# Optimization experiments

Measured on AMD Instinct MI355X. Metric: run time of the kernel, lower is better.

Reference implementation:

```python
import jax, jax.numpy as jnp
import numpy as np

# Dims
B, S, D, N, K, NOPS = 4, 2048, 512, 16, 4, 4
NUM_LAYERS = 1
SCALE = 1.0 / float(np.sqrt(NUM_LAYERS))   # base_layer.residual_scale
GAMMA = 0.01                                # lindblad_gamma
COND_THRESH = 100.0                         # condition_threshold
MHC_ITERS, MHC_TAU = 10, 0.05


def setup_inputs() -> dict:
    key = jax.random.key(0)
    ks = jax.random.split(key, 16)
    def rn(k, shape, s=0.02):
        return jax.random.normal(k, shape, dtype=jnp.float32) * s
    return {
        "x_real": jax.random.normal(ks[0], (B, S, D), dtype=jnp.float32),
        "x_imag": jax.random.normal(ks[1], (B, S, D), dtype=jnp.float32),
        "Win_r": rn(ks[2], (D, D)), "Win_i": rn(ks[3], (D, D)),
        "conv_w": rn(ks[4], (K, D), 0.5),
        "W_dt": rn(ks[5], (D, D)), "b_dt": jnp.full((D,), -4.0, jnp.float32),
        "A_log": jnp.tile(jnp.log(jnp.arange(1, N + 1, dtype=jnp.float32)), (D, 1)),
        "W_B": rn(ks[6], (D, N)), "W_C": rn(ks[7], (D, N)),
        "D_skip": jnp.ones((D,), jnp.float32),
        "Wout_r": rn(ks[8], (D, D)), "Wout_i": rn(ks[9], (D, D)),
        "L_r": rn(ks[10], (NOPS, D), 0.1), "L_i": rn(ks[11], (NOPS, D), 0.1),
        "phi": rn(ks[12], (D,), 0.1),
        "H_res_logits": jnp.zeros((1, 1), jnp.float32),
        "H_res_logits_imag": jnp.zeros((1, 1), jnp.float32),
    }


def _causal_dwconv(u, w):
    # u: [B,S,D] complex, w: [K,D] real depthwise causal kernel
    Kk, Ss = w.shape[0], u.shape[1]
    up = jnp.pad(u, ((0, 0), (Kk - 1, 0), (0, 0)))
    return sum(w[k][None, None, :] * up[:, k:k + Ss, :] for k in range(Kk))


def _forward(x_real, x_imag, Win_r, Win_i, conv_w, W_dt, b_dt, A_log, W_B, W_C,
             D_skip, Wout_r, Wout_i, L_r, L_i, phi, H_res_logits, H_res_logits_imag):
    x = jax.lax.complex(x_real, x_imag)                       # [B,S,D] complex64
    # ---- base ComplexMamba3Layer: complex in-proj -> causal dwconv -> mod-gate -> selective scan -> out-proj ----
    u = x @ jax.lax.complex(Win_r, Win_i)
    u = _causal_dwconv(u, conv_w)
    u = u * jax.nn.sigmoid(jnp.abs(u)).astype(u.dtype)        # magnitude gate (modSiLU)
    xr = u.real
    dt = jax.nn.softplus(xr @ W_dt + b_dt)                    # [B,S,D]
    Bm = xr @ W_B                                             # [B,S,N]
    Cm = xr @ W_C                                             # [B,S,N]
    A = -jnp.exp(A_log)                                       # [D,N]
    def step(h, inp):
        dt_t, Bm_t, Cm_t, u_t = inp                            # [B,D],[B,N],[B,N],[B,D]c
        decay = jnp.exp(dt_t[..., None] * A).astype(h.dtype)  # [B,D,N]
        h = decay * h + (dt_t.astype(u_t.dtype) * u_t)[..., None] * Bm_t[:, None, :].astype(u_t.dtype)
        y_t = jnp.einsum('bdn,bn->bd', h, Cm_t.astype(h.dtype))
        return h, y_t
    h0 = jnp.zeros((x.shape[0], D, N), dtype=u.dtype)
    xs = (jnp.swapaxes(dt, 0, 1), jnp.swapaxes(Bm, 0, 1), jnp.swapaxes(Cm, 0, 1), jnp.swapaxes(u, 0, 1))
    _, ys = jax.lax.scan(step, h0, xs)
    y = jnp.swapaxes(ys, 0, 1) + D_skip.astype(u.dtype) * u
    y = y @ jax.lax.complex(Wout_r, Wout_i)
    out = x + SCALE * y
    # ---- V8 wrapper ----
    branch = (out - x) / max(SCALE, 1e-8)
    # Lindblad dissipation: psi * (1 - gamma * sum_k |L_k|^2), diagonal jump operators
    coeff = jnp.sum(L_r ** 2 + L_i ** 2, axis=0)              # [D]
    branch = branch * (1.0 - GAMMA * coeff).astype(branch.dtype)
    # approximate Hamiltonian (no-grad): H = (1/S) sum_s |psi_s><psi_s|
    mag = jnp.abs(branch)
    H = jax.lax.stop_gradient(jnp.einsum('bsd,bse->bde', mag, mag) / mag.shape[1])
    # hybrid automata: _H_prev is None on the first forward -> no jump applied (faithful to source)
    # quaternionic escape: condition proxy from H diagonal, phase rotation if singular
    diag = jnp.diagonal(H, axis1=1, axis2=2)                  # [B,D]
    cond = jnp.max(diag, axis=-1) / (jnp.min(diag, axis=-1) + 1e-8)
    escaped = cond > COND_THRESH                              # [B]
    rot = jnp.exp(jax.lax.complex(jnp.zeros_like(phi), phi))  # unit phase per dim
    branch = jnp.where(escaped[:, None, None], branch * rot, branch)
    branch = branch * SCALE
    # mHC residual: Sinkhorn on 1x1 logits (streams=1) with complex phase
    M = jnp.exp(H_res_logits / MHC_TAU)
    for _ in range(MHC_ITERS):
        M = M / jnp.sum(M, axis=1, keepdims=True)
        M = M / jnp.sum(M, axis=0, keepdims=True)
    coef = M[0, 0] * jnp.exp(jax.lax.complex(jnp.zeros(()), H_res_logits_imag[0, 0]))
    out = x + coef.astype(branch.dtype) * branch
    return jnp.stack([out.real, out.imag])                    # [2,B,S,D] real view


def reference(x_real, x_imag, Win_r, Win_i, conv_w, W_dt, b_dt, A_log, W_B, W_C,
              D_skip, Wout_r, Wout_i, L_r, L_i, phi, H_res_logits, H_res_logits_imag):
    return _forward(x_real, x_imag, Win_r, Win_i, conv_w, W_dt, b_dt, A_log, W_B, W_C,
                    D_skip, Wout_r, Wout_i, L_r, L_i, phi, H_res_logits, H_res_logits_imag)
```

## Files before the change

kernel.cpp:

```cpp
#include <hip/hip_runtime.h>
#include <math.h>

#define BB 4
#define SSEQ 2048
#define DDIM 512
#define NSTATE 16
#define KCONV 4
#define NOPS_ 4
#define GAMMA_ 0.01f
#define CONDT_ 100.0f
#define SCALE_ 1.0f
#define NC 128
#define LC 16

static const size_t BSD = (size_t)BB * SSEQ * DDIM;
static const size_t BSN = (size_t)BB * SSEQ * NSTATE;
static const size_t MIDSZ = (size_t)BB * NC * DDIM * NSTATE;

typedef short short8v __attribute__((ext_vector_type(8)));
typedef float f32x4 __attribute__((ext_vector_type(4)));

__device__ __forceinline__ short f2bf(float x) {
    union { float f; unsigned int u; } v; v.f = x;
    unsigned int u = v.u + 0x7FFFu + ((v.u >> 16) & 1u);
    return (short)(u >> 16);
}
__device__ __forceinline__ short8v cvt8(const float4 a, const float4 b) {
    short8v r;
    r[0] = f2bf(a.x); r[1] = f2bf(a.y); r[2] = f2bf(a.z); r[3] = f2bf(a.w);
    r[4] = f2bf(b.x); r[5] = f2bf(b.y); r[6] = f2bf(b.z); r[7] = f2bf(b.w);
    return r;
}

__global__ __launch_bounds__(256) void convert_weights(
    const float* __restrict__ W0, const float* __restrict__ W1,
    const float* __restrict__ W2, const float* __restrict__ W3,
    const float* __restrict__ W4,
    unsigned short* __restrict__ T0, unsigned short* __restrict__ T1,
    unsigned short* __restrict__ T2, unsigned short* __restrict__ T3,
    unsigned short* __restrict__ T4)
{
    __shared__ float tile[64][65];
    const int n0 = (blockIdx.x & 7) * 64, k0 = (blockIdx.x >> 3) * 64;
    const float* srcs[5] = {W0, W1, W2, W3, W4};
    unsigned short* dsts[5] = {T0, T1, T2, T3, T4};
    #pragma unroll
    for (int m = 0; m < 5; ++m) {
        const float* W = srcs[m];
        unsigned short* T = dsts[m];
        for (int it = 0; it < 16; ++it) {
            const int idx = it * 256 + threadIdx.x;
            const int r = idx >> 6, c = idx & 63;
            tile[r][c] = W[(size_t)(k0 + r) * DDIM + n0 + c];
        }
        __syncthreads();
        for (int it = 0; it < 16; ++it) {
            const int idx = it * 256 + threadIdx.x;
            const int r = idx >> 6, c = idx & 63;
            T[(size_t)(n0 + r) * DDIM + k0 + c] = (unsigned short)f2bf(tile[c][r]);
        }
        __syncthreads();
    }
}

__global__ __launch_bounds__(256) void convert_bc(
    const float* __restrict__ WB, const float* __restrict__ WC,
    unsigned short* __restrict__ WdtT)
{
    const int idx = blockIdx.x * 256 + threadIdx.x;
    const int r = idx >> 9;
    const int k = idx & 511;
    float v = 0.f;
    if (r < 16) v = WB[(size_t)k * NSTATE + r];
    else if (r < 32) v = WC[(size_t)k * NSTATE + (r - 16)];
    WdtT[(size_t)(512 + r) * DDIM + k] = (unsigned short)f2bf(v);
}

template <bool LIND>
__global__ __launch_bounds__(256, 4) void cgemm_mfma(
    const float* __restrict__ Ar, const float* __restrict__ Ai,
    const unsigned short* __restrict__ WTr, const unsigned short* __restrict__ WTi,
    const float* __restrict__ Lr, const float* __restrict__ Li,
    float* __restrict__ Cr, float* __restrict__ Ci)
{
    __shared__ unsigned short Ar_s[64 * 32], Ai_s[64 * 32];
    __shared__ unsigned short Br_s[64 * 32], Bi_s[64 * 32];
    const int q8 = (int)(gridDim.x >> 3);
    const int lg = (blockIdx.x & 7) * q8 + (blockIdx.x >> 3);
    const int col0 = (lg & 7) * 64;
    const int row0 = (lg >> 3) * 64;
    const int tid = threadIdx.x;
    const int lane = tid & 63, wave = tid >> 6;
    const int wm = wave >> 1, wn = wave & 1;
    const int srow = tid >> 2;
    const int q = tid & 3;

    f32x4 accr[2][2], acci[2][2];
    #pragma unroll
    for (int a = 0; a < 2; ++a)
        #pragma unroll
        for (int b = 0; b < 2; ++b) { accr[a][b] = (f32x4)0.f; acci[a][b] = (f32x4)0.f; }

    for (int k0 = 0; k0 < DDIM; k0 += 32) {
        {
            const size_t ab = (size_t)(row0 + srow) * DDIM + k0 + q * 8;
            const float4 r0 = *reinterpret_cast<const float4*>(Ar + ab);
            const float4 r1 = *reinterpret_cast<const float4*>(Ar + ab + 4);
            const float4 i0 = *reinterpret_cast<const float4*>(Ai + ab);
            const float4 i1 = *reinterpret_cast<const float4*>(Ai + ab + 4);
            const int ix = srow * 32 + ((q ^ ((srow >> 1) & 3)) << 3);
            *reinterpret_cast<short8v*>(&Ar_s[ix]) = cvt8(r0, r1);
            *reinterpret_cast<short8v*>(&Ai_s[ix]) = cvt8(i0, i1);
            const size_t wb = (size_t)(col0 + srow) * DDIM + k0 + q * 8;
            *reinterpret_cast<short8v*>(&Br_s[ix]) = *reinterpret_cast<const short8v*>(WTr + wb);
            *reinterpret_cast<short8v*>(&Bi_s[ix]) = *reinterpret_cast<const short8v*>(WTi + wb);
        }
        __syncthreads();
        short8v ar[2], ai[2], ain[2], wr[2], wi[2];
        const int ks = lane >> 4;
        #pragma unroll
        for (int mi = 0; mi < 2; ++mi) {
            const int r = wm * 32 + mi * 16 + (lane & 15);
            const int idx = r * 32 + ((ks ^ ((r >> 1) & 3)) << 3);
            ar[mi] = *reinterpret_cast<const short8v*>(&Ar_s[idx]);
            ai[mi] = *reinterpret_cast<const short8v*>(&Ai_s[idx]);
            #pragma unroll
            for (int j = 0; j < 8; ++j) ain[mi][j] = ai[mi][j] ^ (short)0x8000;
        }
        #pragma unroll
        for (int nj = 0; nj < 2; ++nj) {
            const int n = wn * 32 + nj * 16 + (lane & 15);
            const int idx = n * 32 + ((ks ^ ((n >> 1) & 3)) << 3);
            wr[nj] = *reinterpret_cast<const short8v*>(&Br_s[idx]);
            wi[nj] = *reinterpret_cast<const short8v*>(&Bi_s[idx]);
        }
        #pragma unroll
        for (int mi = 0; mi < 2; ++mi)
            #pragma unroll
            for (int nj = 0; nj < 2; ++nj) {
                accr[mi][nj] = __builtin_amdgcn_mfma_f32_16x16x32_bf16(ar[mi], wr[nj], accr[mi][nj], 0, 0, 0);
                accr[mi][nj] = __builtin_amdgcn_mfma_f32_16x16x32_bf16(ain[mi], wi[nj], accr[mi][nj], 0, 0, 0);
                acci[mi][nj] = __builtin_amdgcn_mfma_f32_16x16x32_bf16(ar[mi], wi[nj], acci[mi][nj], 0, 0, 0);
                acci[mi][nj] = __builtin_amdgcn_mfma_f32_16x16x32_bf16(ai[mi], wr[nj], acci[mi][nj], 0, 0, 0);
            }
        __syncthreads();
    }
    float lindv[2] = {1.f, 1.f};
    if (LIND) {
        #pragma unroll
        for (int nj = 0; nj < 2; ++nj) {
            const int col = col0 + wn * 32 + nj * 16 + (lane & 15);
            float s = 0.f;
            #pragma unroll
            for (int k = 0; k < NOPS_; ++k) {
                const float lr = Lr[k * DDIM + col], li = Li[k * DDIM + col];
                s += lr * lr + li * li;
            }
            lindv[nj] = 1.0f - GAMMA_ * s;
        }
    }
    #pragma unroll
    for (int mi = 0; mi < 2; ++mi)
        #pragma unroll
        for (int nj = 0; nj < 2; ++nj) {
            const int col = col0 + wn * 32 + nj * 16 + (lane & 15);
            #pragma unroll
            for (int rr = 0; rr < 4; ++rr) {
                const int row = row0 + wm * 32 + mi * 16 + (lane >> 4) * 4 + rr;
                Cr[(size_t)row * DDIM + col] = accr[mi][nj][rr] * lindv[nj];
                Ci[(size_t)row * DDIM + col] = acci[mi][nj][rr] * lindv[nj];
            }
        }
}

__global__ __launch_bounds__(256, 4) void rgemm_fused(
    const float* __restrict__ A, const unsigned short* __restrict__ WT,
    const float* __restrict__ bias, float* __restrict__ Out,
    float* __restrict__ Bm, float* __restrict__ Cm)
{
    __shared__ unsigned short A_s[64 * 32], B_s[64 * 32];
    const int q8 = (int)(gridDim.x >> 3);
    const int lg = (blockIdx.x & 7) * q8 + (blockIdx.x >> 3);
    const int col0 = (lg % 9) * 64;
    const int row0 = (lg / 9) * 64;
    const int tid = threadIdx.x;
    const int lane = tid & 63, wave = tid >> 6;
    const int wm = wave >> 1, wn = wave & 1;
    const int srow = tid >> 2, q = tid & 3;

    f32x4 acc[2][2];
    #pragma unroll
    for (int a = 0; a < 2; ++a)
        #pragma unroll
        for (int b = 0; b < 2; ++b) acc[a][b] = (f32x4)0.f;

    for (int k0 = 0; k0 < DDIM; k0 += 32) {
        {
            const size_t ab = (size_t)(row0 + srow) * DDIM + k0 + q * 8;
            const float4 r0 = *reinterpret_cast<const float4*>(A + ab);
            const float4 r1 = *reinterpret_cast<const float4*>(A + ab + 4);
            const int ix = srow * 32 + ((q ^ ((srow >> 1) & 3)) << 3);
            *reinterpret_cast<short8v*>(&A_s[ix]) = cvt8(r0, r1);
            const size_t wb = (size_t)(col0 + srow) * DDIM + k0 + q * 8;
            *reinterpret_cast<short8v*>(&B_s[ix]) = *reinterpret_cast<const short8v*>(WT + wb);
        }
        __syncthreads();
        short8v av[2], bv[2];
        const int ks = lane >> 4;
        #pragma unroll
        for (int mi = 0; mi < 2; ++mi) {
            const int r = wm * 32 + mi * 16 + (lane & 15);
            av[mi] = *reinterpret_cast<const short8v*>(&A_s[r * 32 + ((ks ^ ((r >> 1) & 3)) << 3)]);
        }
        #pragma unroll
        for (int nj = 0; nj < 2; ++nj) {
            const int n = wn * 32 + nj * 16 + (lane & 15);
            bv[nj] = *reinterpret_cast<const short8v*>(&B_s[n * 32 + ((ks ^ ((n >> 1) & 3)) << 3)]);
        }
        #pragma unroll
        for (int mi = 0; mi < 2; ++mi)
            #pragma unroll
            for (int nj = 0; nj < 2; ++nj)
                acc[mi][nj] = __builtin_amdgcn_mfma_f32_16x16x32_bf16(av[mi], bv[nj], acc[mi][nj], 0, 0, 0);
        __syncthreads();
    }
    #pragma unroll
    for (int mi = 0; mi < 2; ++mi)
        #pragma unroll
        for (int nj = 0; nj < 2; ++nj) {
            const int col = col0 + wn * 32 + nj * 16 + (lane & 15);
            if (col < 512) {
                const float bz = bias[col];
                #pragma unroll
                for (int rr = 0; rr < 4; ++rr) {
                    const int row = row0 + wm * 32 + mi * 16 + (lane >> 4) * 4 + rr;
                    const float z = acc[mi][nj][rr] + bz;
                    Out[(size_t)row * DDIM + col] =
                        (z > 0.f) ? (z + __logf(1.f + __expf(-z))) : __logf(1.f + __expf(z));
                }
            } else if (col < 528) {
                #pragma unroll
                for (int rr = 0; rr < 4; ++rr) {
                    const int row = row0 + wm * 32 + mi * 16 + (lane >> 4) * 4 + rr;
                    Bm[(size_t)row * NSTATE + (col - 512)] = acc[mi][nj][rr];
                }
            } else if (col < 544) {
                #pragma unroll
                for (int rr = 0; rr < 4; ++rr) {
                    const int row = row0 + wm * 32 + mi * 16 + (lane >> 4) * 4 + rr;
                    Cm[(size_t)row * NSTATE + (col - 528)] = acc[mi][nj][rr];
                }
            }
        }
}

__global__ __launch_bounds__(256) void conv_gate_kernel(
    const float* __restrict__ ur, const float* __restrict__ ui,
    const float* __restrict__ w, float* __restrict__ gr, float* __restrict__ gi)
{
    const size_t idx = ((size_t)blockIdx.x * 256 + threadIdx.x) * 4;
    const int d = (int)(idx % DDIM);
    const int s = (int)((idx / DDIM) % SSEQ);
    float4 ar = {0.f, 0.f, 0.f, 0.f}, ai = {0.f, 0.f, 0.f, 0.f};
    #pragma unroll
    for (int k = 0; k < KCONV; ++k) {
        const int soff = s + k - (KCONV - 1);
        if (soff >= 0) {
            const size_t j = idx + (size_t)((long)(k - (KCONV - 1)) * DDIM);
            const float4 wk = *reinterpret_cast<const float4*>(w + k * DDIM + d);
            const float4 u4 = *reinterpret_cast<const float4*>(ur + j);
            const float4 v4 = *reinterpret_cast<const float4*>(ui + j);
            ar.x += wk.x * u4.x; ar.y += wk.y * u4.y; ar.z += wk.z * u4.z; ar.w += wk.w * u4.w;
            ai.x += wk.x * v4.x; ai.y += wk.y * v4.y; ai.z += wk.z * v4.z; ai.w += wk.w * v4.w;
        }
    }
    float4 go_r, go_i;
    {
        const float m0 = sqrtf(ar.x * ar.x + ai.x * ai.x);
        const float m1 = sqrtf(ar.y * ar.y + ai.y * ai.y);
        const float m2 = sqrtf(ar.z * ar.z + ai.z * ai.z);
        const float m3 = sqrtf(ar.w * ar.w + ai.w * ai.w);
        const float s0 = 1.f / (1.f + __expf(-m0));
        const float s1 = 1.f / (1.f + __expf(-m1));
        const float s2 = 1.f / (1.f + __expf(-m2));
        const float s3 = 1.f / (1.f + __expf(-m3));
        go_r.x = ar.x * s0; go_r.y = ar.y * s1; go_r.z = ar.z * s2; go_r.w = ar.w * s3;
        go_i.x = ai.x * s0; go_i.y = ai.y * s1; go_i.z = ai.z * s2; go_i.w = ai.w * s3;
    }
    *reinterpret_cast<float4*>(gr + idx) = go_r;
    *reinterpret_cast<float4*>(gi + idx) = go_i;
}

__global__ __launch_bounds__(256) void scan_phase1(
    const float* __restrict__ dt, const float* __restrict__ gr, const float* __restrict__ gi,
    const float* __restrict__ Bm, const float* __restrict__ A_log,
    float* __restrict__ mid_hr, float* __restrict__ mid_hi, float* __restrict__ dtsum)
{
    __shared__ float bm_s[LC * NSTATE];
    const int blk = blockIdx.x;
    const int dblk = blk & 1;
    const int c = (blk >> 1) & (NC - 1);
    const int b = blk >> 8;
    const int tid = threadIdx.x;
    const int d = dblk * 256 + tid;
    const int s0 = c * LC;
    bm_s[tid] = Bm[((size_t)b * SSEQ + s0) * NSTATE + tid];
    float A_dn[16], hr[16], hi[16];
    #pragma unroll
    for (int n = 0; n < 16; ++n) {
        A_dn[n] = -__expf(A_log[d * NSTATE + n]);
        hr[n] = 0.f; hi[n] = 0.f;
    }
    float dts = 0.f;
    __syncthreads();
    const size_t gbase = (size_t)b * SSEQ * DDIM + (size_t)s0 * DDIM + d;
    for (int i = 0; i < LC; ++i) {
        const float dtv = dt[gbase + (size_t)i * DDIM];
        const float ur = gr[gbase + (size_t)i * DDIM];
        const float ui = gi[gbase + (size_t)i * DDIM];
        dts += dtv;
        const float xr = dtv * ur, xi = dtv * ui;
        #pragma unroll
        for (int n = 0; n < 16; ++n) {
            const float a = __expf(dtv * A_dn[n]);
            const float bmv = bm_s[i * 16 + n];
            hr[n] = a * hr[n] + xr * bmv;
            hi[n] = a * hi[n] + xi * bmv;
        }
    }
    const size_t mbase = ((size_t)(b * NC + c) * DDIM + d) * NSTATE;
    #pragma unroll
    for (int n = 0; n < 16; ++n) { mid_hr[mbase + n] = hr[n]; mid_hi[mbase + n] = hi[n]; }
    dtsum[(size_t)(b * NC + c) * DDIM + d] = dts;
}

__global__ __launch_bounds__(256) void scan_phase2(
    float* __restrict__ mid_hr, float* __restrict__ mid_hi,
    const float* __restrict__ dtsum, const float* __restrict__ A_log)
{
    const int gid = blockIdx.x * 256 + threadIdx.x;
    const int n = gid & 15;
    const int d = (gid >> 4) & (DDIM - 1);
    const int b = gid >> 13;
    const float A_dn = -__expf(A_log[d * NSTATE + n]);
    float hr = 0.f, hi = 0.f;
    for (int c = 0; c < NC; ++c) {
        const size_t cb = (size_t)(b * NC + c) * DDIM + d;
        const float mr = mid_hr[cb * NSTATE + n];
        const float mi = mid_hi[cb * NSTATE + n];
        mid_hr[cb * NSTATE + n] = hr;
        mid_hi[cb * NSTATE + n] = hi;
        const float P = __expf(A_dn * dtsum[cb]);
        hr = mr + P * hr;
        hi = mi + P * hi;
    }
}

__global__ __launch_bounds__(256) void scan_phase3(
    const float* __restrict__ dt, const float* __restrict__ gr, const float* __restrict__ gi,
    const float* __restrict__ Bm, const float* __restrict__ Cm,
    const float* __restrict__ A_log, const float* __restrict__ D_skip,
    const float* __restrict__ hinit_r, const float* __restrict__ hinit_i,
    float* __restrict__ yr, float* __restrict__ yi)
{
    __shared__ float bm_s[LC * NSTATE], cm_s[LC * NSTATE];
    const int blk = blockIdx.x;
    const int dblk = blk & 1;
    const int c = (blk >> 1) & (NC - 1);
    const int b = blk >> 8;
    const int tid = threadIdx.x;
    const int d = dblk * 256 + tid;
    const int s0 = c * LC;
    {
        const size_t base = ((size_t)b * SSEQ + s0) * NSTATE;
        bm_s[tid] = Bm[base + tid];
        cm_s[tid] = Cm[base + tid];
    }
    float A_dn[16], hr[16], hi[16];
    const size_t mbase = ((size_t)(b * NC + c) * DDIM + d) * NSTATE;
    #pragma unroll
    for (int n = 0; n < 16; ++n) {
        A_dn[n] = -__expf(A_log[d * NSTATE + n]);
        hr[n] = hinit_r[mbase + n];
        hi[n] = hinit_i[mbase + n];
    }
    const float dsk = D_skip[d];
    __syncthreads();
    const size_t gbase = (size_t)b * SSEQ * DDIM + (size_t)s0 * DDIM + d;
    for (int i = 0; i < LC; ++i) {
        const float dtv = dt[gbase + (size_t)i * DDIM];
        const float ur = gr[gbase + (size_t)i * DDIM];
        const float ui = gi[gbase + (size_t)i * DDIM];
        const float xr = dtv * ur, xi = dtv * ui;
        float accr = dsk * ur, acci = dsk * ui;
        #pragma unroll
        for (int n = 0; n < 16; ++n) {
            const float a = __expf(dtv * A_dn[n]);
            const float bmv = bm_s[i * 16 + n], cmv = cm_s[i * 16 + n];
            hr[n] = a * hr[n] + xr * bmv;
            hi[n] = a * hi[n] + xi * bmv;
            accr += hr[n] * cmv;
            acci += hi[n] * cmv;
        }
        yr[gbase + (size_t)i * DDIM] = accr;
        yi[gbase + (size_t)i * DDIM] = acci;
    }
}

__global__ __launch_bounds__(256) void diag_kernel(
    const float* __restrict__ br, const float* __restrict__ bi, float* __restrict__ diag)
{
    const int b = blockIdx.x >> 6;
    const int s0 = (blockIdx.x & 63) * 32;
    const int t = threadIdx.x;
    float a0 = 0.f, a1 = 0.f;
    for (int i = 0; i < 32; ++i) {
        const size_t g = (size_t)b * SSEQ * DDIM + (size_t)(s0 + i) * DDIM;
        const float r0 = br[g + t], i0 = bi[g + t];
        const float r1 = br[g + t + 256], i1 = bi[g + t + 256];
        a0 += r0 * r0 + i0 * i0;
        a1 += r1 * r1 + i1 * i1;
    }
    const float inv = 1.0f / (float)SSEQ;
    atomicAdd(&diag[b * DDIM + t], a0 * inv);
    atomicAdd(&diag[b * DDIM + t + 256], a1 * inv);
}

__global__ __launch_bounds__(256) void escape_kernel(
    const float* __restrict__ diag, const float* __restrict__ phi,
    const float* __restrict__ logit, const float* __restrict__ logit_im,
    float* __restrict__ misc, float* __restrict__ rot_r, float* __restrict__ rot_i)
{
    const int tid = threadIdx.x;
    rot_r[tid] = cosf(phi[tid]);
    rot_i[tid] = sinf(phi[tid]);
    rot_r[tid + 256] = cosf(phi[tid + 256]);
    rot_i[tid + 256] = sinf(phi[tid + 256]);
    const int b = tid >> 6, lane = tid & 63;
    float mx = -1e30f, mn = 1e30f;
    for (int j = lane; j < DDIM; j += 64) {
        const float v = diag[b * DDIM + j];
        mx = fmaxf(mx, v);
        mn = fminf(mn, v);
    }
    #pragma unroll
    for (int off = 32; off; off >>= 1) {
        mx = fmaxf(mx, __shfl_xor(mx, off));
        mn = fminf(mn, __shfl_xor(mn, off));
    }
    if (lane == 0) {
        const float cond = mx / (mn + 1e-8f);
        misc[b] = (cond > CONDT_) ? 1.0f : 0.0f;
    }
    if (tid == 0) {
        float M = expf(logit[0] / 0.05f);
        for (int it = 0; it < 10; ++it) { M = M / M; M = M / M; }
        const float im = logit_im[0];
        misc[4] = M * cosf(im);
        misc[5] = M * sinf(im);
    }
}

__global__ __launch_bounds__(256) void final_kernel(
    const float* __restrict__ xr, const float* __restrict__ xi,
    const float* __restrict__ br, const float* __restrict__ bi,
    const float* __restrict__ misc, const float* __restrict__ rot_r,
    const float* __restrict__ rot_i, float* __restrict__ out)
{
    const size_t idx = ((size_t)blockIdx.x * 256 + threadIdx.x) * 4;
    const int d = (int)(idx % DDIM);
    const int b = (int)(idx / ((size_t)SSEQ * DDIM));
    float4 r = *reinterpret_cast<const float4*>(br + idx);
    float4 im = *reinterpret_cast<const float4*>(bi + idx);
    if (misc[b] != 0.0f) {
        const float4 rr = *reinterpret_cast<const float4*>(rot_r + d);
        const float4 ri = *reinterpret_cast<const float4*>(rot_i + d);
        float4 nr, ni;
        nr.x = r.x * rr.x - im.x * ri.x; ni.x = r.x * ri.x + im.x * rr.x;
        nr.y = r.y * rr.y - im.y * ri.y; ni.y = r.y * ri.y + im.y * rr.y;
        nr.z = r.z * rr.z - im.z * ri.z; ni.z = r.z * ri.z + im.z * rr.z;
        nr.w = r.w * rr.w - im.w * ri.w; ni.w = r.w * ri.w + im.w * rr.w;
        r = nr; im = ni;
    }
    const float cr = misc[4] * SCALE_, ci = misc[5] * SCALE_;
    const float4 x4 = *reinterpret_cast<const float4*>(xr + idx);
    const float4 y4 = *reinterpret_cast<const float4*>(xi + idx);
    float4 o0, o1;
    o0.x = x4.x + r.x * cr - im.x * ci; o1.x = y4.x + im.x * cr + r.x * ci;
    o0.y = x4.y + r.y * cr - im.y * ci; o1.y = y4.y + im.y * cr + r.y * ci;
    o0.z = x4.z + r.z * cr - im.z * ci; o1.z = y4.z + im.z * cr + r.z * ci;
    o0.w = x4.w + r.w * cr - im.w * ci; o1.w = y4.w + im.w * cr + r.w * ci;
    *reinterpret_cast<float4*>(out + idx) = o0;
    *reinterpret_cast<float4*>(out + BSD + idx) = o1;
}

extern "C" void kernel_launch(void* const* d_in, const int* in_sizes, int n_in,
                              void* d_out, int out_size, void* d_ws, size_t ws_size,
                              hipStream_t stream)
{
    (void)in_sizes; (void)n_in; (void)out_size; (void)ws_size;
    const float* x_r    = (const float*)d_in[0];
    const float* x_i    = (const float*)d_in[1];
    const float* Win_r  = (const float*)d_in[2];
    const float* Win_i  = (const float*)d_in[3];
    const float* convw  = (const float*)d_in[4];
    const float* W_dt   = (const float*)d_in[5];
    const float* b_dt   = (const float*)d_in[6];
    const float* A_log  = (const float*)d_in[7];
    const float* W_B    = (const float*)d_in[8];
    const float* W_C    = (const float*)d_in[9];
    const float* D_skip = (const float*)d_in[10];
    const float* Wout_r = (const float*)d_in[11];
    const float* Wout_i = (const float*)d_in[12];
    const float* L_r    = (const float*)d_in[13];
    const float* L_i    = (const float*)d_in[14];
    const float* phi    = (const float*)d_in[15];
    const float* hres   = (const float*)d_in[16];
    const float* hresi  = (const float*)d_in[17];
    float* out = (float*)d_out;

    float* f    = (float*)d_ws;
    float* u_r  = f;
    float* u_i  = f + BSD;
    float* g_r  = f + 2 * BSD;
    float* g_i  = f + 3 * BSD;
    float* dt   = f + 4 * BSD;
    float* y_r  = f + 5 * BSD;
    float* y_i  = f + 6 * BSD;
    float* Bm   = f + 7 * BSD;
    float* Cm   = Bm + BSN;
    float* dtsum = Cm + BSN;
    float* diag = dtsum + (size_t)BB * NC * DDIM;
    float* misc = diag + (size_t)BB * DDIM;
    float* rot_r = misc + 8;
    float* rot_i = rot_r + DDIM;
    unsigned short* wbase = (unsigned short*)(rot_i + DDIM);
    unsigned short* WinT_r  = wbase;
    unsigned short* WinT_i  = wbase + 1 * 262144;
    unsigned short* WoutT_r = wbase + 2 * 262144;
    unsigned short* WoutT_i = wbase + 3 * 262144;
    unsigned short* WdtT    = wbase + 4 * 262144;
    float* mid_hr  = u_r;
    float* mid_hi  = u_i;
    float* br_r = u_r;
    float* br_i = u_i;

    convert_weights<<<64, 256, 0, stream>>>(Win_r, Win_i, Wout_r, Wout_i, W_dt,
                                            WinT_r, WinT_i, WoutT_r, WoutT_i, WdtT);
    convert_bc<<<128, 256, 0, stream>>>(W_B, W_C, WdtT);
    cgemm_mfma<false><<<1024, 256, 0, stream>>>(
        x_r, x_i, WinT_r, WinT_i, nullptr, nullptr, u_r, u_i);
    conv_gate_kernel<<<(int)(BSD / 1024), 256, 0, stream>>>(u_r, u_i, convw, g_r, g_i);
    rgemm_fused<<<1152, 256, 0, stream>>>(g_r, WdtT, b_dt, dt, Bm, Cm);
    scan_phase1<<<BB * NC * 2, 256, 0, stream>>>(dt, g_r, g_i, Bm, A_log, mid_hr, mid_hi, dtsum);
    scan_phase2<<<128, 256, 0, stream>>>(mid_hr, mid_hi, dtsum, A_log);
    scan_phase3<<<BB * NC * 2, 256, 0, stream>>>(dt, g_r, g_i, Bm, Cm, A_log, D_skip,
                                                 mid_hr, mid_hi, y_r, y_i);
    cgemm_mfma<true><<<1024, 256, 0, stream>>>(
        y_r, y_i, WoutT_r, WoutT_i, L_r, L_i, br_r, br_i);
    hipMemsetAsync(diag, 0, (size_t)BB * DDIM * sizeof(float), stream);
    diag_kernel<<<256, 256, 0, stream>>>(br_r, br_i, diag);
    escape_kernel<<<1, 256, 0, stream>>>(diag, phi, hres, hresi, misc, rot_r, rot_i);
    final_kernel<<<(int)(BSD / 1024), 256, 0, stream>>>(
        x_r, x_i, br_r, br_i, misc, rot_r, rot_i, out);
}
```

Baseline: 332.6 us.

## Double-buffer LDS tiles in complex and real MFMA GEMMs with register prefetch

Both GEMM kernels now keep two shared-memory tile buffers. Each iteration issues the global loads for the next K-tile into registers before running the MFMAs on the current tile, then writes them to the alternate buffer. This needs one barrier per iteration instead of two and overlaps global memory latency with compute. In exchange, shared memory use doubles and the prefetched values need more registers, which may reduce occupancy under the launch bounds of 256 threads and 4 blocks.

```diff
diff --git a/kernel.cpp b/kernel.cpp
--- a/kernel.cpp
+++ b/kernel.cpp
@@ -83,8 +83,8 @@
     const float* __restrict__ Lr, const float* __restrict__ Li,
     float* __restrict__ Cr, float* __restrict__ Ci)
 {
-    __shared__ unsigned short Ar_s[64 * 32], Ai_s[64 * 32];
-    __shared__ unsigned short Br_s[64 * 32], Bi_s[64 * 32];
+    __shared__ unsigned short Ar_s[2][64 * 32], Ai_s[2][64 * 32];
+    __shared__ unsigned short Br_s[2][64 * 32], Bi_s[2][64 * 32];
     const int q8 = (int)(gridDim.x >> 3);
     const int lg = (blockIdx.x & 7) * q8 + (blockIdx.x >> 3);
     const int col0 = (lg & 7) * 64;
@@ -94,6 +94,9 @@
     const int wm = wave >> 1, wn = wave & 1;
     const int srow = tid >> 2;
     const int q = tid & 3;
+    const size_t abase = (size_t)(row0 + srow) * DDIM + q * 8;
+    const size_t wbase = (size_t)(col0 + srow) * DDIM + q * 8;
+    const int ix = srow * 32 + ((q ^ ((srow >> 1) & 3)) << 3);
 
     f32x4 accr[2][2], acci[2][2];
     #pragma unroll
@@ -101,29 +104,40 @@
         #pragma unroll
         for (int b = 0; b < 2; ++b) { accr[a][b] = (f32x4)0.f; acci[a][b] = (f32x4)0.f; }
 
-    for (int k0 = 0; k0 < DDIM; k0 += 32) {
-        {
-            const size_t ab = (size_t)(row0 + srow) * DDIM + k0 + q * 8;
-            const float4 r0 = *reinterpret_cast<const float4*>(Ar + ab);
-            const float4 r1 = *reinterpret_cast<const float4*>(Ar + ab + 4);
-            const float4 i0 = *reinterpret_cast<const float4*>(Ai + ab);
-            const float4 i1 = *reinterpret_cast<const float4*>(Ai + ab + 4);
-            const int ix = srow * 32 + ((q ^ ((srow >> 1) & 3)) << 3);
-            *reinterpret_cast<short8v*>(&Ar_s[ix]) = cvt8(r0, r1);
-            *reinterpret_cast<short8v*>(&Ai_s[ix]) = cvt8(i0, i1);
-            const size_t wb = (size_t)(col0 + srow) * DDIM + k0 + q * 8;
-            *reinterpret_cast<short8v*>(&Br_s[ix]) = *reinterpret_cast<const short8v*>(WTr + wb);
-            *reinterpret_cast<short8v*>(&Bi_s[ix]) = *reinterpret_cast<const short8v*>(WTi + wb);
-        }
-        __syncthreads();
+    {
+        const float4 r0 = *reinterpret_cast<const float4*>(Ar + abase);
+        const float4 r1 = *reinterpret_cast<const float4*>(Ar + abase + 4);
+        const float4 i0 = *reinterpret_cast<const float4*>(Ai + abase);
+        const float4 i1 = *reinterpret_cast<const float4*>(Ai + abase + 4);
+        *reinterpret_cast<short8v*>(&Ar_s[0][ix]) = cvt8(r0, r1);
+        *reinterpret_cast<short8v*>(&Ai_s[0][ix]) = cvt8(i0, i1);
+        *reinterpret_cast<short8v*>(&Br_s[0][ix]) = *reinterpret_cast<const short8v*>(WTr + wbase);
+        *reinterpret_cast<short8v*>(&Bi_s[0][ix]) = *reinterpret_cast<const short8v*>(WTi + wbase);
+    }
+    __syncthreads();
+
+    for (int kt = 0; kt < 16; ++kt) {
+        const int cur = kt & 1;
+        float4 nr0, nr1, ni0, ni1;
+        short8v nwr, nwi;
+        if (kt < 15) {
+            const size_t ab = abase + (size_t)(kt + 1) * 32;
+            nr0 = *reinterpret_cast<const float4*>(Ar + ab);
+            nr1 = *reinterpret_cast<const float4*>(Ar + ab + 4);
+            ni0 = *reinterpret_cast<const float4*>(Ai + ab);
+            ni1 = *reinterpret_cast<const float4*>(Ai + ab + 4);
+            const size_t wb = wbase + (size_t)(kt + 1) * 32;
+            nwr = *reinterpret_cast<const short8v*>(WTr + wb);
+            nwi = *reinterpret_cast<const short8v*>(WTi + wb);
+        }
         short8v ar[2], ai[2], ain[2], wr[2], wi[2];
         const int ks = lane >> 4;
         #pragma unroll
         for (int mi = 0; mi < 2; ++mi) {
             const int r = wm * 32 + mi * 16 + (lane & 15);
             const int idx = r * 32 + ((ks ^ ((r >> 1) & 3)) << 3);
-            ar[mi] = *reinterpret_cast<const short8v*>(&Ar_s[idx]);
-            ai[mi] = *reinterpret_cast<const short8v*>(&Ai_s[idx]);
+            ar[mi] = *reinterpret_cast<const short8v*>(&Ar_s[cur][idx]);
+            ai[mi] = *reinterpret_cast<const short8v*>(&Ai_s[cur][idx]);
             #pragma unroll
             for (int j = 0; j < 8; ++j) ain[mi][j] = ai[mi][j] ^ (short)0x8000;
         }
@@ -131,8 +145,8 @@
         for (int nj = 0; nj < 2; ++nj) {
             const int n = wn * 32 + nj * 16 + (lane & 15);
             const int idx = n * 32 + ((ks ^ ((n >> 1) & 3)) << 3);
-            wr[nj] = *reinterpret_cast<const short8v*>(&Br_s[idx]);
-            wi[nj] = *reinterpret_cast<const short8v*>(&Bi_s[idx]);
+            wr[nj] = *reinterpret_cast<const short8v*>(&Br_s[cur][idx]);
+            wi[nj] = *reinterpret_cast<const short8v*>(&Bi_s[cur][idx]);
         }
         #pragma unroll
         for (int mi = 0; mi < 2; ++mi)
@@ -143,6 +157,12 @@
                 acci[mi][nj] = __builtin_amdgcn_mfma_f32_16x16x32_bf16(ar[mi], wi[nj], acci[mi][nj], 0, 0, 0);
                 acci[mi][nj] = __builtin_amdgcn_mfma_f32_16x16x32_bf16(ai[mi], wr[nj], acci[mi][nj], 0, 0, 0);
             }
+        if (kt < 15) {
+            *reinterpret_cast<short8v*>(&Ar_s[cur ^ 1][ix]) = cvt8(nr0, nr1);
+            *reinterpret_cast<short8v*>(&Ai_s[cur ^ 1][ix]) = cvt8(ni0, ni1);
+            *reinterpret_cast<short8v*>(&Br_s[cur ^ 1][ix]) = nwr;
+            *reinterpret_cast<short8v*>(&Bi_s[cur ^ 1][ix]) = nwi;
+        }
         __syncthreads();
     }
     float lindv[2] = {1.f, 1.f};
@@ -178,7 +198,7 @@
     const float* __restrict__ bias, float* __restrict__ Out,
     float* __restrict__ Bm, float* __restrict__ Cm)
 {
-    __shared__ unsigned short A_s[64 * 32], B_s[64 * 32];
+    __shared__ unsigned short A_s[2][64 * 32], B_s[2][64 * 32];
     const int q8 = (int)(gridDim.x >> 3);
     const int lg = (blockIdx.x & 7) * q8 + (blockIdx.x >> 3);
     const int col0 = (lg % 9) * 64;
@@ -187,6 +207,9 @@
     const int lane = tid & 63, wave = tid >> 6;
     const int wm = wave >> 1, wn = wave & 1;
     const int srow = tid >> 2, q = tid & 3;
+    const size_t abase = (size_t)(row0 + srow) * DDIM + q * 8;
+    const size_t wbase = (size_t)(col0 + srow) * DDIM + q * 8;
+    const int ix = srow * 32 + ((q ^ ((srow >> 1) & 3)) << 3);
 
     f32x4 acc[2][2];
     #pragma unroll
@@ -194,34 +217,45 @@
         #pragma unroll
         for (int b = 0; b < 2; ++b) acc[a][b] = (f32x4)0.f;
 
-    for (int k0 = 0; k0 < DDIM; k0 += 32) {
-        {
-            const size_t ab = (size_t)(row0 + srow) * DDIM + k0 + q * 8;
-            const float4 r0 = *reinterpret_cast<const float4*>(A + ab);
-            const float4 r1 = *reinterpret_cast<const float4*>(A + ab + 4);
-            const int ix = srow * 32 + ((q ^ ((srow >> 1) & 3)) << 3);
-            *reinterpret_cast<short8v*>(&A_s[ix]) = cvt8(r0, r1);
-            const size_t wb = (size_t)(col0 + srow) * DDIM + k0 + q * 8;
-            *reinterpret_cast<short8v*>(&B_s[ix]) = *reinterpret_cast<const short8v*>(WT + wb);
-        }
-        __syncthreads();
+    {
+        const float4 r0 = *reinterpret_cast<const float4*>(A + abase);
+        const float4 r1 = *reinterpret_cast<const float4*>(A + abase + 4);
+        *reinterpret_cast<short8v*>(&A_s[0][ix]) = cvt8(r0, r1);
+        *reinterpret_cast<short8v*>(&B_s[0][ix]) = *reinterpret_cast<const short8v*>(WT + wbase);
+    }
+    __syncthreads();
+
+    for (int kt = 0; kt < 16; ++kt) {
+        const int cur = kt & 1;
+        float4 nr0, nr1;
+        short8v nw;
+        if (kt < 15) {
+            const size_t ab = abase + (size_t)(kt + 1) * 32;
+            nr0 = *reinterpret_cast<const float4*>(A + ab);
+            nr1 = *reinterpret_cast<const float4*>(A + ab + 4);
+            nw = *reinterpret_cast<const short8v*>(WT + wbase + (size_t)(kt + 1) * 32);
+        }
         short8v av[2], bv[2];
         const int ks = lane >> 4;
         #pragma unroll
         for (int mi = 0; mi < 2; ++mi) {
             const int r = wm * 32 + mi * 16 + (lane & 15);
-            av[mi] = *reinterpret_cast<const short8v*>(&A_s[r * 32 + ((ks ^ ((r >> 1) & 3)) << 3)]);
+            av[mi] = *reinterpret_cast<const short8v*>(&A_s[cur][r * 32 + ((ks ^ ((r >> 1) & 3)) << 3)]);
         }
         #pragma unroll
         for (int nj = 0; nj < 2; ++nj) {
             const int n = wn * 32 + nj * 16 + (lane & 15);
-            bv[nj] = *reinterpret_cast<const short8v*>(&B_s[n * 32 + ((ks ^ ((n >> 1) & 3)) << 3)]);
+            bv[nj] = *reinterpret_cast<const short8v*>(&B_s[cur][n * 32 + ((ks ^ ((n >> 1) & 3)) << 3)]);
         }
         #pragma unroll
         for (int mi = 0; mi < 2; ++mi)
             #pragma unroll
             for (int nj = 0; nj < 2; ++nj)
                 acc[mi][nj] = __builtin_amdgcn_mfma_f32_16x16x32_bf16(av[mi], bv[nj], acc[mi][nj], 0, 0, 0);
+        if (kt < 15) {
+            *reinterpret_cast<short8v*>(&A_s[cur ^ 1][ix]) = cvt8(nr0, nr1);
+            *reinterpret_cast<short8v*>(&B_s[cur ^ 1][ix]) = nw;
+        }
         __syncthreads();
     }
     #pragma unroll
```

Result: no change. 331.4 us (-0.4%).
